# Performance work log

Hardware: AMD Instinct MI355X
Metric: run time of the kernel (lower is better)

The kernel has to match this reference:

```python
import jax, jax.numpy as jnp
import numpy as np


def setup_inputs() -> dict:
    key = jax.random.key(0)
    n_samples, n_points, dims = 16, 2048, 64
    h = jax.random.normal(key, (n_samples, n_points, dims), dtype=jnp.float32)
    return {"h": h, "K": 16}


def reference(h, K):
    """Pairwise squared distance + K nearest neighbors -> edge list.

    h : (n_samples, n_points, dims)
    Returns (knn_dist, dst, src):
      knn_dist : (n_samples, n_points, K) squared distances to the K nearest points
      dst, src : (n_samples*n_points*K,) int32 globally-offset edge endpoints
    """
    n_samples, n_points, _ = h.shape
    # d[b, i, j] = ||h[b,i]||^2 + ||h[b,j]||^2 - 2 <h[b,i], h[b,j]>
    x2s = jnp.sum(h * h, axis=-1, keepdims=True)          # (s, n, 1)
    d = x2s + jnp.swapaxes(x2s, -1, -2) - 2.0 * jnp.einsum('bnd,bmd->bnm', h, h)
    # smallest-K == top-K of negated distances (matches torch.topk largest=False order)
    neg_vals, k_indices = jax.lax.top_k(-d, K)            # (s, n, K)
    knn_dist = -neg_vals
    # edge list with per-sample node-id offsets (matches the torch flattening)
    src = jnp.broadcast_to(jnp.arange(n_points, dtype=k_indices.dtype)[None, :, None],
                           k_indices.shape)
    offset = (jnp.arange(n_samples, dtype=k_indices.dtype) * n_points)[:, None, None]
    dst = (k_indices + offset).reshape(-1)
    src = (src + offset).reshape(-1)
    return knn_dist, dst, src
```

## Files before the change

kernel.cpp:

```cpp
#include <hip/hip_runtime.h>
#include <hip/hip_fp16.h>
#include <cfloat>


typedef _Float16 half8 __attribute__((ext_vector_type(8)));
typedef _Float16 half4 __attribute__((ext_vector_type(4)));
typedef float    f32x4 __attribute__((ext_vector_type(4)));

constexpr int NS = 16, NP = 2048, ND = 64, KK = 16;
constexpr int NWV = 4;
constexpr int NT  = NWV * 64;
constexpr int RB  = 32;
constexpr int ITN = RB / 16;
constexpr int JW  = NP / NWV;
constexpr int NJT = JW / 16;
constexpr int PF  = 4;
constexpr int MS  = 17;
constexpr int RCAP = 128;
constexpr int RSTR = RCAP + 1;
constexpr float MARGIN = 1.0f;

__global__ __launch_bounds__(256)
void prep_kernel(const float* __restrict__ h, float* __restrict__ x2,
                 _Float16* __restrict__ hh)
{
    const int b = blockIdx.x;
    const int t = threadIdx.x;
    const size_t base = (size_t)b * 16 * ND;

    float4 v = *(const float4*)(h + base + (size_t)t * 4);
    half4 p;
    p[0] = (_Float16)v.x; p[1] = (_Float16)v.y;
    p[2] = (_Float16)v.z; p[3] = (_Float16)v.w;
    *(half4*)(hh + base + (size_t)t * 4) = p;

    if (t < 16) {
        const int g = b * 16 + t;
        const float4* row = (const float4*)(h + (size_t)g * ND);
        const int ph = g & 15;
        float a0 = 0.f, a1 = 0.f, a2 = 0.f, a3 = 0.f;
        #pragma unroll
        for (int k = 0; k < 16; ++k) {
            float4 u = row[(k + ph) & 15];
            a0 = fmaf(u.x, u.x, a0); a1 = fmaf(u.y, u.y, a1);
            a2 = fmaf(u.z, u.z, a2); a3 = fmaf(u.w, u.w, a3);
        }
        x2[g] = (a0 + a1) + (a2 + a3);
    }
}

__device__ __forceinline__ bool lexlt(float a, int ja, float b, int jb)
{
    return (a < b) || (a == b && ja < jb);
}
__device__ __forceinline__ void insert16x(float (&d)[KK], int (&ix)[KK],
                                          float v, int j)
{
    #pragma unroll
    for (int p = KK - 1; p > 0; --p) {
        bool sh = lexlt(v, j, d[p - 1], ix[p - 1]);
        bool he = lexlt(v, j, d[p], ix[p]);
        float nd = sh ? d[p - 1] : (he ? v : d[p]);
        int   ni = sh ? ix[p - 1] : (he ? j : ix[p]);
        d[p] = nd; ix[p] = ni;
    }
    if (lexlt(v, j, d[0], ix[0])) { d[0] = v; ix[0] = j; }
}

__global__ __launch_bounds__(NT, 4)
void knn_mfma(const float* __restrict__ h, const _Float16* __restrict__ hh,
              const float* __restrict__ x2g, float* __restrict__ out)
{
    __shared__ __align__(16) float smem[8544];
    float* ldsx2  = smem;
    float* mw     = smem + 2048;
    float* ldsthr = smem + 2176;
    int*   rcnt   = (int*)(smem + 2208);
    int*   ring   = (int*)(smem + 2240);
    float* md     = smem + 6368;
    int*   mi     = (int*)(smem + 7456);

    const int t   = threadIdx.x;
    const int ln  = t & 63;
    const int qd  = ln >> 4;
    const int cl  = ln & 15;
    const int q   = t >> 6;
    const int row = ln & 31;
    const int jh  = ln >> 5;
    const int bid = blockIdx.x;
    const int xcd = bid & 7;
    const int kb  = bid >> 3;
    const int s   = xcd + ((kb & 1) << 3);
    const int rb  = kb >> 1;
    const int rowbase = rb * RB;
    const float*    __restrict__ hs  = h  + (size_t)s * NP * ND;
    const _Float16* __restrict__ hhs = hh + (size_t)s * NP * ND;

    ((float4*)ldsx2)[t]       = ((const float4*)(x2g + s * NP))[t];
    ((float4*)ldsx2)[t + 256] = ((const float4*)(x2g + s * NP))[t + 256];
    if (t < RB) rcnt[t] = 0;

    half8 ifr[ITN][2];
    #pragma unroll
    for (int it = 0; it < ITN; ++it) {
        const _Float16* ap = hhs + (size_t)(rowbase + it * 16 + cl) * ND + qd * 8;
        ifr[it][0] = *(const half8*)(ap);
        ifr[it][1] = *(const half8*)(ap + 32);
    }
    __syncthreads();

    const int jbase = q * JW;
    const _Float16* __restrict__ jrow0 = hhs + (size_t)(jbase + cl) * ND + qd * 8;

    auto loadj = [&](int jt, half8 &lo, half8 &hi, f32x4 &xq) {
        const _Float16* bp = jrow0 + (size_t)jt * (16 * ND);
        lo = *(const half8*)(bp);
        hi = *(const half8*)(bp + 32);
        xq = *(const f32x4*)(ldsx2 + jbase + jt * 16 + qd * 4);
    };

    float t1[ITN], t2[ITN], t3[ITN], t4[ITN];
    #pragma unroll
    for (int it = 0; it < ITN; ++it)
        { t1[it] = FLT_MAX; t2[it] = FLT_MAX; t3[it] = FLT_MAX; t4[it] = FLT_MAX; }

    {
        half8 plo[PF], phi[PF]; f32x4 pxq[PF];
        #pragma unroll
        for (int p = 0; p < PF; ++p) loadj(p, plo[p], phi[p], pxq[p]);

        for (int t0 = 0; t0 < NJT; t0 += PF) {
            #pragma unroll
            for (int p = 0; p < PF; ++p) {
                half8 clo = plo[p], chi = phi[p]; f32x4 cxq = pxq[p];
                int nx = t0 + p + PF;
                if (nx < NJT) loadj(nx, plo[p], phi[p], pxq[p]);
                #pragma unroll
                for (int it = 0; it < ITN; ++it) {
                    f32x4 acc;
                    acc = __builtin_amdgcn_mfma_f32_16x16x32_f16(
                              clo, ifr[it][0], (f32x4){0.f, 0.f, 0.f, 0.f}, 0, 0, 0);
                    acc = __builtin_amdgcn_mfma_f32_16x16x32_f16(
                              chi, ifr[it][1], acc, 0, 0, 0);
                    #pragma unroll
                    for (int r = 0; r < 4; ++r) {
                        float v  = fmaf(-2.f, acc[r], cxq[r]);
                        float n1 = fminf(t1[it], v);
                        float n2 = __builtin_amdgcn_fmed3f(t1[it], t2[it], v);
                        float n3 = __builtin_amdgcn_fmed3f(t2[it], t3[it], v);
                        float n4 = __builtin_amdgcn_fmed3f(t3[it], t4[it], v);
                        t1[it] = n1; t2[it] = n2; t3[it] = n3; t4[it] = n4;
                    }
                }
            }
        }
    }

    #pragma unroll
    for (int it = 0; it < ITN; ++it) {
        #pragma unroll
        for (int lvl = 0; lvl < 2; ++lvl) {
            const int mask = 16 << lvl;
            float b1 = __shfl_xor(t1[it], mask), b2 = __shfl_xor(t2[it], mask);
            float b3 = __shfl_xor(t3[it], mask), b4 = __shfl_xor(t4[it], mask);
            float m1 = fminf(t1[it], b4), m2 = fminf(t2[it], b3);
            float m3 = fminf(t3[it], b2), m4 = fminf(t4[it], b1);
            float u1 = fminf(m1, m3), u3 = fmaxf(m1, m3);
            float u2 = fminf(m2, m4), u4 = fmaxf(m2, m4);
            t1[it] = fminf(u1, u2); t2[it] = fmaxf(u1, u2);
            t3[it] = fminf(u3, u4); t4[it] = fmaxf(u3, u4);
        }
    }
    if (qd == 0) {
        mw[q * 32 + cl]      = t4[0];
        mw[q * 32 + 16 + cl] = t4[1];
    }
    __syncthreads();
    if (q == 0 && ln < 32) {
        float m0 = mw[row], m1 = mw[32 + row];
        float m2 = mw[64 + row], m3 = mw[96 + row];
        ldsthr[row] = fmaxf(fmaxf(m0, m1), fmaxf(m2, m3)) + MARGIN;
    }
    __syncthreads();

    float thrv[ITN];
    #pragma unroll
    for (int it = 0; it < ITN; ++it) thrv[it] = ldsthr[it * 16 + cl];

    {
        half8 plo[PF], phi[PF]; f32x4 pxq[PF];
        #pragma unroll
        for (int p = 0; p < PF; ++p) loadj(p, plo[p], phi[p], pxq[p]);

        for (int t0 = 0; t0 < NJT; t0 += PF) {
            #pragma unroll
            for (int p = 0; p < PF; ++p) {
                half8 clo = plo[p], chi = phi[p]; f32x4 cxq = pxq[p];
                const int j0 = jbase + (t0 + p) * 16;
                int nx = t0 + p + PF;
                if (nx < NJT) loadj(nx, plo[p], phi[p], pxq[p]);
                #pragma unroll
                for (int it = 0; it < ITN; ++it) {
                    f32x4 acc;
                    acc = __builtin_amdgcn_mfma_f32_16x16x32_f16(
                              clo, ifr[it][0], (f32x4){0.f, 0.f, 0.f, 0.f}, 0, 0, 0);
                    acc = __builtin_amdgcn_mfma_f32_16x16x32_f16(
                              chi, ifr[it][1], acc, 0, 0, 0);
                    #pragma unroll
                    for (int r = 0; r < 4; ++r) {
                        float d2 = fmaf(-2.f, acc[r], cxq[r]);
                        if (d2 < thrv[it]) {
                            int rw = it * 16 + cl;
                            int slot = atomicAdd(&rcnt[rw], 1);
                            if (slot < RCAP) ring[rw * RSTR + slot] = j0 + qd * 4 + r;
                        }
                    }
                }
            }
        }
    }
    __syncthreads();

    const int myrow = rowbase + row;
    float4 A[16];
    {
        const float4* ra = (const float4*)(hs + (size_t)myrow * ND);
        #pragma unroll
        for (int k = 0; k < 16; ++k) A[k] = ra[k];
    }
    float x2i;
    {
        float a0 = 0.f, a1 = 0.f, a2 = 0.f, a3 = 0.f;
        #pragma unroll
        for (int k = 0; k < 16; ++k) {
            a0 = fmaf(A[k].x, A[k].x, a0); a1 = fmaf(A[k].y, A[k].y, a1);
            a2 = fmaf(A[k].z, A[k].z, a2); a3 = fmaf(A[k].w, A[k].w, a3);
        }
        x2i = (a0 + a1) + (a2 + a3);
    }
    float dist[KK]; int idx[KK];
    #pragma unroll
    for (int k = 0; k < KK; ++k) { dist[k] = FLT_MAX; idx[k] = 0; }

    const int cntR = min(rcnt[row], RCAP);
    const int w8 = q * 2 + jh;
    #pragma unroll 1
    for (int k = w8; k < cntR; k += 8) {
        int j = ring[row * RSTR + k];
        const float4* cv = (const float4*)(hs + (size_t)j * ND);
        float a0 = 0.f, a1 = 0.f, a2 = 0.f, a3 = 0.f;
        #pragma unroll
        for (int kk = 0; kk < 16; ++kk) {
            float4 c = cv[kk];
            a0 = fmaf(A[kk].x, c.x, a0); a1 = fmaf(A[kk].y, c.y, a1);
            a2 = fmaf(A[kk].z, c.z, a2); a3 = fmaf(A[kk].w, c.w, a3);
        }
        float dotv = (a0 + a1) + (a2 + a3);
        float d2 = fmaf(-2.0f, dotv, x2i + ldsx2[j]);
        if (lexlt(d2, j, dist[KK - 1], idx[KK - 1]))
            insert16x(dist, idx, d2, j);
    }

    #pragma unroll 1
    for (int k = 0; k < KK; ++k) {
        float v  = __shfl(dist[k], row + 32);
        int   jv = __shfl(idx[k],  row + 32);
        bool need = (ln < 32) && lexlt(v, jv, dist[KK - 1], idx[KK - 1]);
        if (!__any(need)) break;
        if (need) insert16x(dist, idx, v, jv);
    }
    __syncthreads();
    #pragma unroll 1
    for (int lvl = 0; lvl < 2; ++lvl) {
        const int step = 1 << lvl;
        const int m    = (step << 1) - 1;
        const bool pub = ((q & m) == step) && ln < 32;
        const int reg  = q >> (lvl + 1);
        if (pub) {
            #pragma unroll
            for (int k = 0; k < KK; ++k) {
                md[(reg * RB + row) * MS + k] = dist[k];
                mi[(reg * RB + row) * MS + k] = idx[k];
            }
        }
        __syncthreads();
        if ((q & m) == 0) {
            #pragma unroll 1
            for (int k = 0; k < KK; ++k) {
                float v  = md[(reg * RB + row) * MS + k];
                int   jv = mi[(reg * RB + row) * MS + k];
                bool need = (ln < 32) && lexlt(v, jv, dist[KK - 1], idx[KK - 1]);
                if (!__any(need)) break;
                if (need) insert16x(dist, idx, v, jv);
            }
        }
        __syncthreads();
    }

    if (q == 0 && ln < 32) {
        const int off = s * NP;
        const size_t rg = (size_t)off + myrow;
        float* o0 = out + rg * KK;
        float* o1 = out + (size_t)NS * NP * KK + rg * KK;
        float* o2 = out + (size_t)2 * NS * NP * KK + rg * KK;
        #pragma unroll
        for (int k = 0; k < KK; ++k) o0[k] = dist[k];
        #pragma unroll
        for (int k = 0; k < KK; ++k) o1[k] = (float)(idx[k] + off);
        #pragma unroll
        for (int k = 0; k < KK; ++k) o2[k] = (float)(off + myrow);
    }
}

extern "C" void kernel_launch(void* const* d_in, const int* in_sizes, int n_in,
                              void* d_out, int out_size, void* d_ws, size_t ws_size,
                              hipStream_t stream)
{
    const float* h = (const float*)d_in[0];
    float* out = (float*)d_out;
    float*    x2 = (float*)d_ws;
    _Float16* hh = (_Float16*)(x2 + NS * NP);

    hipLaunchKernelGGL(prep_kernel, dim3(NS * NP / 16), dim3(256), 0, stream,
                       h, x2, hh);
    hipLaunchKernelGGL(knn_mfma, dim3(NS * (NP / RB)), dim3(NT), 0, stream,
                       h, hh, x2, out);
}
```

Measured before the change: 210.7 us.

## Derive KNN threshold from partial scan and fuse threshold pass with top-4 tracking

The first MFMA pass, which only tracks per-row top-4 distances to set a candidate threshold, now scans only the first 16 tiles. The remaining tiles are scanned once, collecting candidates under that loose threshold while still updating the top-4. A tightened threshold is then used to rescan the first 16 tiles. This replaces a full extra pass over the distance matrix with one partial rescan. Because the early threshold is looser, more candidates land in the ring, so RCAP grows to 176 and a brute-force fallback over all points is added for rows that overflow. The risks are more atomics and refinement work, larger LDS use, and a slow fallback path if overflow happens.

```diff
diff --git a/kernel.cpp b/kernel.cpp
--- a/kernel.cpp
+++ b/kernel.cpp
@@ -14,9 +14,10 @@
 constexpr int ITN = RB / 16;
 constexpr int JW  = NP / NWV;
 constexpr int NJT = JW / 16;
+constexpr int NJT0 = 16;
 constexpr int PF  = 4;
 constexpr int MS  = 17;
-constexpr int RCAP = 128;
+constexpr int RCAP = 176;
 constexpr int RSTR = RCAP + 1;
 constexpr float MARGIN = 1.0f;
 
@@ -67,18 +68,31 @@
     if (lexlt(v, j, d[0], ix[0])) { d[0] = v; ix[0] = j; }
 }
 
+__device__ __forceinline__ void bitonic4(float &a1, float &a2, float &a3,
+                                         float &a4, int mask)
+{
+    float b1 = __shfl_xor(a1, mask), b2 = __shfl_xor(a2, mask);
+    float b3 = __shfl_xor(a3, mask), b4 = __shfl_xor(a4, mask);
+    float m1 = fminf(a1, b4), m2 = fminf(a2, b3);
+    float m3 = fminf(a3, b2), m4 = fminf(a4, b1);
+    float u1 = fminf(m1, m3), u3 = fmaxf(m1, m3);
+    float u2 = fminf(m2, m4), u4 = fmaxf(m2, m4);
+    a1 = fminf(u1, u2); a2 = fmaxf(u1, u2);
+    a3 = fminf(u3, u4); a4 = fmaxf(u3, u4);
+}
+
 __global__ __launch_bounds__(NT, 4)
 void knn_mfma(const float* __restrict__ h, const _Float16* __restrict__ hh,
               const float* __restrict__ x2g, float* __restrict__ out)
 {
-    __shared__ __align__(16) float smem[8544];
+    __shared__ __align__(16) float smem[10080];
     float* ldsx2  = smem;
     float* mw     = smem + 2048;
     float* ldsthr = smem + 2176;
     int*   rcnt   = (int*)(smem + 2208);
     int*   ring   = (int*)(smem + 2240);
-    float* md     = smem + 6368;
-    int*   mi     = (int*)(smem + 7456);
+    float* md     = smem + 7904;
+    int*   mi     = (int*)(smem + 8992);
 
     const int t   = threadIdx.x;
     const int ln  = t & 63;
@@ -123,18 +137,19 @@
     #pragma unroll
     for (int it = 0; it < ITN; ++it)
         { t1[it] = FLT_MAX; t2[it] = FLT_MAX; t3[it] = FLT_MAX; t4[it] = FLT_MAX; }
+    float thrv[ITN];
 
     {
         half8 plo[PF], phi[PF]; f32x4 pxq[PF];
         #pragma unroll
         for (int p = 0; p < PF; ++p) loadj(p, plo[p], phi[p], pxq[p]);
 
-        for (int t0 = 0; t0 < NJT; t0 += PF) {
+        for (int t0 = 0; t0 < NJT0; t0 += PF) {
             #pragma unroll
             for (int p = 0; p < PF; ++p) {
                 half8 clo = plo[p], chi = phi[p]; f32x4 cxq = pxq[p];
                 int nx = t0 + p + PF;
-                if (nx < NJT) loadj(nx, plo[p], phi[p], pxq[p]);
+                if (nx < NJT0) loadj(nx, plo[p], phi[p], pxq[p]);
                 #pragma unroll
                 for (int it = 0; it < ITN; ++it) {
                     f32x4 acc;
@@ -156,24 +171,20 @@
         }
     }
 
-    #pragma unroll
-    for (int it = 0; it < ITN; ++it) {
-        #pragma unroll
-        for (int lvl = 0; lvl < 2; ++lvl) {
-            const int mask = 16 << lvl;
-            float b1 = __shfl_xor(t1[it], mask), b2 = __shfl_xor(t2[it], mask);
-            float b3 = __shfl_xor(t3[it], mask), b4 = __shfl_xor(t4[it], mask);
-            float m1 = fminf(t1[it], b4), m2 = fminf(t2[it], b3);
-            float m3 = fminf(t3[it], b2), m4 = fminf(t4[it], b1);
-            float u1 = fminf(m1, m3), u3 = fmaxf(m1, m3);
-            float u2 = fminf(m2, m4), u4 = fmaxf(m2, m4);
-            t1[it] = fminf(u1, u2); t2[it] = fmaxf(u1, u2);
-            t3[it] = fminf(u3, u4); t4[it] = fmaxf(u3, u4);
-        }
-    }
-    if (qd == 0) {
-        mw[q * 32 + cl]      = t4[0];
-        mw[q * 32 + 16 + cl] = t4[1];
+    {
+        float c1[ITN], c2[ITN], c3[ITN], c4[ITN];
+        #pragma unroll
+        for (int it = 0; it < ITN; ++it)
+            { c1[it] = t1[it]; c2[it] = t2[it]; c3[it] = t3[it]; c4[it] = t4[it]; }
+        #pragma unroll
+        for (int it = 0; it < ITN; ++it) {
+            bitonic4(c1[it], c2[it], c3[it], c4[it], 16);
+            bitonic4(c1[it], c2[it], c3[it], c4[it], 32);
+        }
+        if (qd == 0) {
+            mw[q * 32 + cl]      = c4[0];
+            mw[q * 32 + 16 + cl] = c4[1];
+        }
     }
     __syncthreads();
     if (q == 0 && ln < 32) {
@@ -182,23 +193,78 @@
         ldsthr[row] = fmaxf(fmaxf(m0, m1), fmaxf(m2, m3)) + MARGIN;
     }
     __syncthreads();
-
-    float thrv[ITN];
     #pragma unroll
     for (int it = 0; it < ITN; ++it) thrv[it] = ldsthr[it * 16 + cl];
 
     {
         half8 plo[PF], phi[PF]; f32x4 pxq[PF];
         #pragma unroll
-        for (int p = 0; p < PF; ++p) loadj(p, plo[p], phi[p], pxq[p]);
-
-        for (int t0 = 0; t0 < NJT; t0 += PF) {
+        for (int p = 0; p < PF; ++p) loadj(NJT0 + p, plo[p], phi[p], pxq[p]);
+
+        for (int t0 = NJT0; t0 < NJT; t0 += PF) {
             #pragma unroll
             for (int p = 0; p < PF; ++p) {
                 half8 clo = plo[p], chi = phi[p]; f32x4 cxq = pxq[p];
                 const int j0 = jbase + (t0 + p) * 16;
                 int nx = t0 + p + PF;
                 if (nx < NJT) loadj(nx, plo[p], phi[p], pxq[p]);
+                #pragma unroll
+                for (int it = 0; it < ITN; ++it) {
+                    f32x4 acc;
+                    acc = __builtin_amdgcn_mfma_f32_16x16x32_f16(
+                              clo, ifr[it][0], (f32x4){0.f, 0.f, 0.f, 0.f}, 0, 0, 0);
+                    acc = __builtin_amdgcn_mfma_f32_16x16x32_f16(
+                              chi, ifr[it][1], acc, 0, 0, 0);
+                    #pragma unroll
+                    for (int r = 0; r < 4; ++r) {
+                        float v  = fmaf(-2.f, acc[r], cxq[r]);
+                        if (v < thrv[it]) {
+                            int rw = it * 16 + cl;
+                            int slot = atomicAdd(&rcnt[rw], 1);
+                            if (slot < RCAP) ring[rw * RSTR + slot] = j0 + qd * 4 + r;
+                        }
+                        float n1 = fminf(t1[it], v);
+                        float n2 = __builtin_amdgcn_fmed3f(t1[it], t2[it], v);
+                        float n3 = __builtin_amdgcn_fmed3f(t2[it], t3[it], v);
+                        float n4 = __builtin_amdgcn_fmed3f(t3[it], t4[it], v);
+                        t1[it] = n1; t2[it] = n2; t3[it] = n3; t4[it] = n4;
+                    }
+                }
+            }
+        }
+    }
+
+    #pragma unroll
+    for (int it = 0; it < ITN; ++it) {
+        bitonic4(t1[it], t2[it], t3[it], t4[it], 16);
+        bitonic4(t1[it], t2[it], t3[it], t4[it], 32);
+    }
+    if (qd == 0) {
+        mw[q * 32 + cl]      = t4[0];
+        mw[q * 32 + 16 + cl] = t4[1];
+    }
+    __syncthreads();
+    if (q == 0 && ln < 32) {
+        float m0 = mw[row], m1 = mw[32 + row];
+        float m2 = mw[64 + row], m3 = mw[96 + row];
+        ldsthr[row] = fmaxf(fmaxf(m0, m1), fmaxf(m2, m3)) + MARGIN;
+    }
+    __syncthreads();
+    #pragma unroll
+    for (int it = 0; it < ITN; ++it) thrv[it] = ldsthr[it * 16 + cl];
+
+    {
+        half8 plo[PF], phi[PF]; f32x4 pxq[PF];
+        #pragma unroll
+        for (int p = 0; p < PF; ++p) loadj(p, plo[p], phi[p], pxq[p]);
+
+        for (int t0 = 0; t0 < NJT0; t0 += PF) {
+            #pragma unroll
+            for (int p = 0; p < PF; ++p) {
+                half8 clo = plo[p], chi = phi[p]; f32x4 cxq = pxq[p];
+                const int j0 = jbase + (t0 + p) * 16;
+                int nx = t0 + p + PF;
+                if (nx < NJT0) loadj(nx, plo[p], phi[p], pxq[p]);
                 #pragma unroll
                 for (int it = 0; it < ITN; ++it) {
                     f32x4 acc;
@@ -242,23 +308,41 @@
     #pragma unroll
     for (int k = 0; k < KK; ++k) { dist[k] = FLT_MAX; idx[k] = 0; }
 
-    const int cntR = min(rcnt[row], RCAP);
+    const int rawc = rcnt[row];
     const int w8 = q * 2 + jh;
-    #pragma unroll 1
-    for (int k = w8; k < cntR; k += 8) {
-        int j = ring[row * RSTR + k];
-        const float4* cv = (const float4*)(hs + (size_t)j * ND);
-        float a0 = 0.f, a1 = 0.f, a2 = 0.f, a3 = 0.f;
-        #pragma unroll
-        for (int kk = 0; kk < 16; ++kk) {
-            float4 c = cv[kk];
-            a0 = fmaf(A[kk].x, c.x, a0); a1 = fmaf(A[kk].y, c.y, a1);
-            a2 = fmaf(A[kk].z, c.z, a2); a3 = fmaf(A[kk].w, c.w, a3);
-        }
-        float dotv = (a0 + a1) + (a2 + a3);
-        float d2 = fmaf(-2.0f, dotv, x2i + ldsx2[j]);
-        if (lexlt(d2, j, dist[KK - 1], idx[KK - 1]))
-            insert16x(dist, idx, d2, j);
+    if (rawc <= RCAP) {
+        #pragma unroll 1
+        for (int k = w8; k < rawc; k += 8) {
+            int j = ring[row * RSTR + k];
+            const float4* cv = (const float4*)(hs + (size_t)j * ND);
+            float a0 = 0.f, a1 = 0.f, a2 = 0.f, a3 = 0.f;
+            #pragma unroll
+            for (int kk = 0; kk < 16; ++kk) {
+                float4 c = cv[kk];
+                a0 = fmaf(A[kk].x, c.x, a0); a1 = fmaf(A[kk].y, c.y, a1);
+                a2 = fmaf(A[kk].z, c.z, a2); a3 = fmaf(A[kk].w, c.w, a3);
+            }
+            float dotv = (a0 + a1) + (a2 + a3);
+            float d2 = fmaf(-2.0f, dotv, x2i + ldsx2[j]);
+            if (lexlt(d2, j, dist[KK - 1], idx[KK - 1]))
+                insert16x(dist, idx, d2, j);
+        }
+    } else {
+        #pragma unroll 1
+        for (int j = w8; j < NP; j += 8) {
+            const float4* cv = (const float4*)(hs + (size_t)j * ND);
+            float a0 = 0.f, a1 = 0.f, a2 = 0.f, a3 = 0.f;
+            #pragma unroll
+            for (int kk = 0; kk < 16; ++kk) {
+                float4 c = cv[kk];
+                a0 = fmaf(A[kk].x, c.x, a0); a1 = fmaf(A[kk].y, c.y, a1);
+                a2 = fmaf(A[kk].z, c.z, a2); a3 = fmaf(A[kk].w, c.w, a3);
+            }
+            float dotv = (a0 + a1) + (a2 + a3);
+            float d2 = fmaf(-2.0f, dotv, x2i + ldsx2[j]);
+            if (lexlt(d2, j, dist[KK - 1], idx[KK - 1]))
+                insert16x(dist, idx, d2, j);
+        }
     }
 
     #pragma unroll 1
```

Result: slower. 236.1 us (+12.0%).
